# Performance work log

Hardware: AMD Instinct MI355X
Metric: run time of the kernel (lower is better)

## Reference

```python
import math
import jax, jax.numpy as jnp
import numpy as np

B, L, D, H = 4, 1024, 1024, 16
HD = D // H  # head_dim = 64


def rel_pos_embed(seq_len: int, dim: int, padding_idx: int = 0) -> jnp.ndarray:
    """RelativeSinusoidalPositionalEmbedding for seq_len > origin_shift case:
    table regenerated with num_embeddings = 2*seq_len, origin_shift = seq_len,
    positions = arange(-L, L) + L selects the full table. Returns [2L, dim]."""
    num = 2 * seq_len
    half = dim // 2
    scale = math.log(10000.0) / (half - 1)
    freq = np.exp(np.arange(half, dtype=np.float32) * -scale)
    pos = np.arange(-num // 2, num // 2, dtype=np.float32)
    emb = pos[:, None] * freq[None, :]                      # [2L, half]
    emb = np.concatenate([np.sin(emb), np.cos(emb)], axis=1).astype(np.float32)
    emb[padding_idx] = 0.0
    return jnp.asarray(emb)


def _shift(BD):
    """Transformer-XL shift: [b,n,L,2L] -> [b,n,L,L] aligning relative positions."""
    b, n, l, _ = BD.shape
    zero_pad = jnp.zeros((b, n, l, 1), BD.dtype)
    BD = jnp.concatenate([BD, zero_pad], axis=-1).reshape(b, n, -1, l)  # [b,n,2L+1,L]
    BD = BD[:, :, : 2 * l].reshape(b, n, l, -1)                          # [b,n,L,2L]
    return BD[..., l:]                                                    # [b,n,L,L]


def setup_inputs() -> dict:
    key = jax.random.key(0)
    k0, k1, k2, k3 = jax.random.split(key, 4)
    x = jax.random.normal(k0, (B, L, D), jnp.float32)
    Wqv = jax.random.normal(k1, (D, 2 * D), jnp.float32) * (1.0 / math.sqrt(D))
    r_r_bias = jax.random.normal(k2, (H, HD), jnp.float32) * 0.1
    r_w_bias = jax.random.normal(k3, (H, HD), jnp.float32) * 0.1
    mask = jnp.ones((B, L), jnp.int32)
    return {"x": x, "Wqv": Wqv, "r_r_bias": r_r_bias, "r_w_bias": r_w_bias, "mask": mask}


def reference(x, Wqv, r_r_bias, r_w_bias, mask):
    b, l, d = x.shape
    pos = rel_pos_embed(l, HD)                               # [2L, HD] (detached buffer)
    qv = x @ Wqv                                             # [b, L, 2D]
    q, v = jnp.split(qv, 2, axis=-1)
    q = q.reshape(b, l, H, HD).transpose(0, 2, 1, 3)         # [b, H, L, HD]
    v = v.reshape(b, l, H, HD).transpose(0, 2, 1, 3)
    k = x.reshape(b, l, H, HD).transpose(0, 2, 1, 3)         # k_as_x=True: k is x reshaped

    rw_head_q = q + r_r_bias[None, :, None, :]
    AC = jnp.einsum('bnqd,bnkd->bnqk', rw_head_q, k)         # [b,H,L,L]
    D_ = jnp.einsum('nd,ld->nl', r_w_bias, pos)[None, :, None, :]  # [1,H,1,2L]
    B_ = jnp.einsum('bnqd,ld->bnql', q, pos)                 # [b,H,L,2L]
    BD = _shift(B_ + D_)                                     # [b,H,L,L]

    attn = AC + BD
    attn = jnp.where(mask[:, None, None, :] == 0, -jnp.inf, attn)
    attn = jax.nn.softmax(attn, axis=-1)                     # dropout is identity (eval)
    out = jnp.einsum('bnqk,bnkd->bnqd', attn, v)
    return out.transpose(0, 2, 1, 3).reshape(b, l, d)
```

## Files before the change

### kernel.cpp

```cpp
#include <hip/hip_runtime.h>
#include <hip/hip_bf16.h>
#include <math.h>


typedef __attribute__((ext_vector_type(8))) short short8;
typedef __attribute__((ext_vector_type(4))) short short4v;
typedef __attribute__((ext_vector_type(4))) float f32x4;

#define MFMA16(a,b,c) __builtin_amdgcn_mfma_f32_16x16x32_bf16(a,b,c,0,0,0)

__device__ __forceinline__ short f2bf(float f) {
  union { float f; unsigned int u; } v; v.f = f;
  unsigned int u = v.u;
  u += 0x7FFFu + ((u >> 16) & 1u);
  return (short)(u >> 16);
}
__device__ __forceinline__ float bf2f(short h) {
  union { unsigned int u; float f; } v;
  v.u = ((unsigned int)(unsigned short)h) << 16;
  return v.f;
}
__device__ __forceinline__ void glds16(const short* g, short* l) {
  __builtin_amdgcn_global_load_lds(
      (const __attribute__((address_space(1))) void*)g,
      (__attribute__((address_space(3))) void*)l, 16, 0, 0);
}

__global__ __launch_bounds__(256) void k_trig(float* __restrict__ T) {
  int idx = blockIdx.x * 256 + threadIdx.x;
  int l = idx >> 6, c = idx & 63, cc = c & 31;
  float fr = (float)exp(-(double)cc * 0.2971077539347156);
  double ang = (double)l * (double)fr;
  T[idx] = (float)((c < 32) ? sin(ang) : cos(ang));
}

__global__ __launch_bounds__(256) void k_split_x(const float* __restrict__ x,
    short* __restrict__ xh, short* __restrict__ xl) {
  int i = blockIdx.x * 256 + threadIdx.x;
  f32x4 v = ((const f32x4*)x)[i];
  short4v h, l;
#pragma unroll
  for (int c = 0; c < 4; ++c) {
    short hb = f2bf(v[c]);
    h[c] = hb;
    l[c] = f2bf(v[c] - bf2f(hb));
  }
  ((short4v*)xh)[i] = h;
  ((short4v*)xl)[i] = l;
}

__global__ __launch_bounds__(256) void k_wt(const float* __restrict__ W,
    short* __restrict__ wth, short* __restrict__ wtl) {
  __shared__ __align__(16) float tile[64*65];
  int n0 = blockIdx.x * 64, k0 = blockIdx.y * 64;
  int tid = threadIdx.x;
#pragma unroll
  for (int i = 0; i < 16; ++i) {
    int e = tid + i*256, r = e >> 6, c = e & 63;
    tile[r*65 + c] = W[(k0 + r)*2048 + n0 + c];
  }
  __syncthreads();
#pragma unroll
  for (int i = 0; i < 16; ++i) {
    int e = tid + i*256, r = e >> 6, c = e & 63;
    float v = tile[c*65 + r];
    short hb = f2bf(v);
    wth[(n0 + r)*1024 + k0 + c] = hb;
    wtl[(n0 + r)*1024 + k0 + c] = f2bf(v - bf2f(hb));
  }
}

#define LDK 40
__global__ __launch_bounds__(256) void k_gemm(
    const short* __restrict__ xh, const short* __restrict__ xl,
    const short* __restrict__ wth, const short* __restrict__ wtl,
    float* __restrict__ qf, short* __restrict__ vbt) {
  __shared__ __align__(16) short Ah[128*LDK], Al[128*LDK], Bh[128*LDK], Bl[128*LDK];
  int tid = threadIdx.x;
  int m0 = blockIdx.x * 128, n0 = blockIdx.y * 128;
  int lane = tid & 63, w = tid >> 6;
  int wm = w >> 1, wn = w & 1;
  int g = lane >> 4, lr = lane & 15;
  f32x4 acc[4][4] = {};
  for (int kt = 0; kt < 32; ++kt) {
    int k0 = kt * 32;
#pragma unroll
    for (int i = 0; i < 2; ++i) {
      int L = tid + i*256;
      int r = L >> 2, c8 = (L & 3) * 8;
      *(short8*)&Ah[r*LDK + c8] = *(const short8*)&xh[(m0+r)*1024 + k0 + c8];
      *(short8*)&Al[r*LDK + c8] = *(const short8*)&xl[(m0+r)*1024 + k0 + c8];
      *(short8*)&Bh[r*LDK + c8] = *(const short8*)&wth[(n0+r)*1024 + k0 + c8];
      *(short8*)&Bl[r*LDK + c8] = *(const short8*)&wtl[(n0+r)*1024 + k0 + c8];
    }
    __syncthreads();
    short8 ah[4], al[4], bh[4], bl[4];
#pragma unroll
    for (int mf = 0; mf < 4; ++mf) {
      int row = wm*64 + mf*16 + lr;
      ah[mf] = *(short8*)&Ah[row*LDK + g*8];
      al[mf] = *(short8*)&Al[row*LDK + g*8];
    }
#pragma unroll
    for (int nf = 0; nf < 4; ++nf) {
      int row = wn*64 + nf*16 + lr;
      bh[nf] = *(short8*)&Bh[row*LDK + g*8];
      bl[nf] = *(short8*)&Bl[row*LDK + g*8];
    }
#pragma unroll
    for (int mf = 0; mf < 4; ++mf)
#pragma unroll
      for (int nf = 0; nf < 4; ++nf) {
        acc[mf][nf] = MFMA16(ah[mf], bh[nf], acc[mf][nf]);
        acc[mf][nf] = MFMA16(al[mf], bh[nf], acc[mf][nf]);
        acc[mf][nf] = MFMA16(ah[mf], bl[nf], acc[mf][nf]);
      }
    __syncthreads();
  }
#pragma unroll
  for (int mf = 0; mf < 4; ++mf)
#pragma unroll
    for (int nf = 0; nf < 4; ++nf) {
      int row0 = m0 + wm*64 + mf*16 + g*4;
      int col  = n0 + wn*64 + nf*16 + lr;
      if (col < 1024) {
#pragma unroll
        for (int ri = 0; ri < 4; ++ri)
          qf[(row0 + ri)*1024 + col] = acc[mf][nf][ri];
      } else {
        int c2 = col - 1024, h = c2 >> 6, d = c2 & 63;
        int b = row0 >> 10, l0 = row0 & 1023;
        short4v pk;
#pragma unroll
        for (int ri = 0; ri < 4; ++ri) pk[ri] = f2bf(acc[mf][nf][ri]);
        *(short4v*)&vbt[((b*16 + h)*64 + d)*1024 + l0] = pk;
      }
    }
}

__global__ __launch_bounds__(256) void k_qcat(const float* __restrict__ qf,
    const float* __restrict__ rrb, const float* __restrict__ rwb,
    const float* __restrict__ T, short* __restrict__ qch, short* __restrict__ qcl) {
  int row = blockIdx.x * 4 + (threadIdx.x >> 6);
  int lane = threadIdx.x & 63;
  int b = row >> 14, h = (row >> 10) & 15, l = row & 1023;
  float q  = qf[(b*1024 + l)*1024 + h*64 + lane];
  float qa = q + rrb[h*64 + lane];
  float qb = q + rwb[h*64 + lane];
  int c = lane & 31;
  float qs = __shfl(qb, c, 64);
  float qc = __shfl(qb, c + 32, 64);
  float ts = T[l*64 + c];
  float tc = T[l*64 + c + 32];
  float v2 = (lane < 32) ? (qs*tc + qc*ts) : (qc*tc - qs*ts);
  short ha = f2bf(qa), h2 = f2bf(v2);
  qch[row*128 + lane]      = ha;
  qcl[row*128 + lane]      = f2bf(qa - bf2f(ha));
  qch[row*128 + 64 + lane] = h2;
  qcl[row*128 + 64 + lane] = f2bf(v2 - bf2f(h2));
}

__global__ __launch_bounds__(256) void k_kcat(const float* __restrict__ x,
    const float* __restrict__ T, short* __restrict__ kch, short* __restrict__ kcl) {
  int row = blockIdx.x * 4 + (threadIdx.x >> 6);
  int lane = threadIdx.x & 63;
  int b = row >> 14, h = (row >> 10) & 15, k = row & 1023;
  float xv = x[(b*1024 + k)*1024 + h*64 + lane];
  float tv = T[k*64 + lane];
  short hx = f2bf(xv), ht = f2bf(tv);
  int sw = k & 7;
  int c0 = lane, c1 = 64 + lane;
  int p0 = ((((c0 >> 3) ^ sw) << 3) | (c0 & 7));
  int p1 = ((((c1 >> 3) ^ sw) << 3) | (c1 & 7));
  kch[row*128 + p0] = hx;
  kcl[row*128 + p0] = f2bf(xv - bf2f(hx));
  kch[row*128 + p1] = ht;
  kcl[row*128 + p1] = f2bf(tv - bf2f(ht));
}

#define NKT 32
#define PLDW 40
__global__ __launch_bounds__(512, 4) void k_attn(
    const short* __restrict__ qch, const short* __restrict__ qcl,
    const short* __restrict__ kch, const short* __restrict__ kcl,
    const short* __restrict__ vbt, float* __restrict__ out) {
  __shared__ __align__(16) short Kh[2][32*128], Kl[2][32*128], Pl[8][16*PLDW];
  int tid = threadIdx.x, lane = tid & 63, w = tid >> 6;
  int g = lane >> 4, lr = lane & 15;
  int id = blockIdx.x;
  int s = id >> 3, xcd = id & 7;
  int bh = xcd*8 + (s & 7), qt = s >> 3;
  int q0 = qt * 128;
  short8 qh[4], ql[4];
  int qrow = bh*1024 + q0 + w*16 + lr;
#pragma unroll
  for (int kc = 0; kc < 4; ++kc) {
    qh[kc] = *(const short8*)&qch[qrow*128 + kc*32 + g*8];
    ql[kc] = *(const short8*)&qcl[qrow*128 + kc*32 + g*8];
  }
  f32x4 o[4] = {};
  float m_run[4], l_run[4];
#pragma unroll
  for (int r = 0; r < 4; ++r) { m_run[r] = -1e30f; l_run[r] = 0.f; }
  short* Pw = &Pl[w][0];
  glds16(&kch[(bh*1024)*128 + tid*8], &Kh[0][tid*8]);
  glds16(&kcl[(bh*1024)*128 + tid*8], &Kl[0][tid*8]);
  __syncthreads();
  for (int kt = 0; kt < NKT; ++kt) {
    int cur = kt & 1;
    short8 vb[4];
#pragma unroll
    for (int df = 0; df < 4; ++df)
      vb[df] = *(const short8*)&vbt[(bh*64 + df*16 + lr)*1024 + kt*32 + g*8];
    if (kt + 1 < NKT) {
      int off = (bh*1024 + (kt+1)*32)*128;
      glds16(&kch[off + tid*8], &Kh[cur^1][tid*8]);
      glds16(&kcl[off + tid*8], &Kl[cur^1][tid*8]);
    }
    f32x4 sacc[2] = {};
#pragma unroll
    for (int kc = 0; kc < 4; ++kc)
#pragma unroll
      for (int nf = 0; nf < 2; ++nf) {
        int boff = (nf*16 + lr)*256 + ((((kc<<2) + g) ^ (lr & 7)) << 4);
        short8 kbh = *(short8*)((char*)&Kh[cur][0] + boff);
        short8 kbl = *(short8*)((char*)&Kl[cur][0] + boff);
        sacc[nf] = MFMA16(qh[kc], kbh, sacc[nf]);
        sacc[nf] = MFMA16(ql[kc], kbh, sacc[nf]);
        sacc[nf] = MFMA16(qh[kc], kbl, sacc[nf]);
      }
    float mt[4];
#pragma unroll
    for (int r = 0; r < 4; ++r) mt[r] = fmaxf(sacc[0][r], sacc[1][r]);
#pragma unroll
    for (int off = 1; off < 16; off <<= 1)
#pragma unroll
      for (int r = 0; r < 4; ++r)
        mt[r] = fmaxf(mt[r], __shfl_xor(mt[r], off, 64));
    float sc[4], rs[4];
#pragma unroll
    for (int r = 0; r < 4; ++r) {
      float mn = fmaxf(m_run[r], mt[r]);
      sc[r] = __expf(m_run[r] - mn);
      m_run[r] = mn;
      rs[r] = 0.f;
    }
#pragma unroll
    for (int nf = 0; nf < 2; ++nf)
#pragma unroll
      for (int r = 0; r < 4; ++r) {
        float p = __expf(sacc[nf][r] - m_run[r]);
        rs[r] += p;
        Pw[(g*4 + r)*PLDW + nf*16 + lr] = f2bf(p);
      }
#pragma unroll
    for (int off = 1; off < 16; off <<= 1)
#pragma unroll
      for (int r = 0; r < 4; ++r)
        rs[r] += __shfl_xor(rs[r], off, 64);
#pragma unroll
    for (int r = 0; r < 4; ++r) l_run[r] = l_run[r]*sc[r] + rs[r];
#pragma unroll
    for (int df = 0; df < 4; ++df)
#pragma unroll
      for (int r = 0; r < 4; ++r)
        o[df][r] *= sc[r];
    short8 pa = *(short8*)&Pw[lr*PLDW + g*8];
#pragma unroll
    for (int df = 0; df < 4; ++df)
      o[df] = MFMA16(pa, vb[df], o[df]);
    __syncthreads();
  }
  int b = bh >> 4, h = bh & 15;
#pragma unroll
  for (int df = 0; df < 4; ++df)
#pragma unroll
    for (int r = 0; r < 4; ++r) {
      int qa = q0 + w*16 + g*4 + r;
      out[(b*1024 + qa)*1024 + h*64 + df*16 + lr] = o[df][r] / l_run[r];
    }
}

extern "C" void kernel_launch(void* const* d_in, const int* in_sizes, int n_in,
                              void* d_out, int out_size, void* d_ws, size_t ws_size,
                              hipStream_t stream) {
  const float* x   = (const float*)d_in[0];
  const float* Wqv = (const float*)d_in[1];
  const float* rrb = (const float*)d_in[2];
  const float* rwb = (const float*)d_in[3];
  float* out = (float*)d_out;
  char* ws = (char*)d_ws;
  const size_t MB = 1u << 20;
  float* T   = (float*)(ws);
  short* vbt = (short*)(ws + 1*MB);
  short* qch = (short*)(ws + 9*MB);
  short* qcl = (short*)(ws + 25*MB);
  short* kch = (short*)(ws + 41*MB);
  short* kcl = (short*)(ws + 57*MB);
  short* xh  = (short*)(ws + 41*MB);
  short* xl  = (short*)(ws + 49*MB);
  short* wth = (short*)(ws + 57*MB);
  short* wtl = (short*)(ws + 61*MB);
  float* qf  = (float*)d_out;

  hipLaunchKernelGGL(k_trig,   dim3(256),      dim3(256), 0, stream, T);
  hipLaunchKernelGGL(k_split_x,dim3(4096),     dim3(256), 0, stream, x, xh, xl);
  hipLaunchKernelGGL(k_wt,     dim3(32, 16),   dim3(256), 0, stream, Wqv, wth, wtl);
  hipLaunchKernelGGL(k_gemm,   dim3(32, 16),   dim3(256), 0, stream, xh, xl, wth, wtl, qf, vbt);
  hipLaunchKernelGGL(k_qcat,   dim3(16384),    dim3(256), 0, stream, qf, rrb, rwb, T, qch, qcl);
  hipLaunchKernelGGL(k_kcat,   dim3(16384),    dim3(256), 0, stream, x, T, kch, kcl);
  hipLaunchKernelGGL(k_attn,   dim3(512),      dim3(512), 0, stream, qch, qcl, kch, kcl, vbt, out);
}
```

Before: 283.4 us.

## Double query rows per wave in attention, lazy rescale, MFMA rowsum, direct LDS loads

The attention kernel now runs 4 waves per block, and each wave handles two 16-row query tiles, so every K fragment read from LDS feeds twice as many MFMAs. Online-softmax rescaling is skipped unless the running max grows by more than a threshold. Row sums are accumulated through an extra MFMA against a ones vector instead of shuffle reductions. The GEMM uses global_load_lds for staging with an unpadded LDS layout, and both kernels raise wave priority around MFMA blocks. The risks are higher register pressure, possible LDS bank conflicts in the unpadded GEMM tiles, and a larger range for the bf16 probabilities.

```diff
diff --git a/kernel.cpp b/kernel.cpp
--- a/kernel.cpp
+++ b/kernel.cpp
@@ -70,12 +70,11 @@
   }
 }
 
-#define LDK 40
 __global__ __launch_bounds__(256) void k_gemm(
     const short* __restrict__ xh, const short* __restrict__ xl,
     const short* __restrict__ wth, const short* __restrict__ wtl,
     float* __restrict__ qf, short* __restrict__ vbt) {
-  __shared__ __align__(16) short Ah[128*LDK], Al[128*LDK], Bh[128*LDK], Bl[128*LDK];
+  __shared__ __align__(16) short Ah[128*32], Al[128*32], Bh[128*32], Bl[128*32];
   int tid = threadIdx.x;
   int m0 = blockIdx.x * 128, n0 = blockIdx.y * 128;
   int lane = tid & 63, w = tid >> 6;
@@ -85,28 +84,29 @@
   for (int kt = 0; kt < 32; ++kt) {
     int k0 = kt * 32;
 #pragma unroll
-    for (int i = 0; i < 2; ++i) {
-      int L = tid + i*256;
-      int r = L >> 2, c8 = (L & 3) * 8;
-      *(short8*)&Ah[r*LDK + c8] = *(const short8*)&xh[(m0+r)*1024 + k0 + c8];
-      *(short8*)&Al[r*LDK + c8] = *(const short8*)&xl[(m0+r)*1024 + k0 + c8];
-      *(short8*)&Bh[r*LDK + c8] = *(const short8*)&wth[(n0+r)*1024 + k0 + c8];
-      *(short8*)&Bl[r*LDK + c8] = *(const short8*)&wtl[(n0+r)*1024 + k0 + c8];
+    for (int p = 0; p < 2; ++p) {
+      int e = p*256 + tid;
+      int r = e >> 2, c8 = (e & 3) * 8, e8 = e * 8;
+      glds16(&xh [(m0+r)*1024 + k0 + c8], &Ah[e8]);
+      glds16(&xl [(m0+r)*1024 + k0 + c8], &Al[e8]);
+      glds16(&wth[(n0+r)*1024 + k0 + c8], &Bh[e8]);
+      glds16(&wtl[(n0+r)*1024 + k0 + c8], &Bl[e8]);
     }
     __syncthreads();
     short8 ah[4], al[4], bh[4], bl[4];
 #pragma unroll
     for (int mf = 0; mf < 4; ++mf) {
       int row = wm*64 + mf*16 + lr;
-      ah[mf] = *(short8*)&Ah[row*LDK + g*8];
-      al[mf] = *(short8*)&Al[row*LDK + g*8];
+      ah[mf] = *(short8*)&Ah[row*32 + g*8];
+      al[mf] = *(short8*)&Al[row*32 + g*8];
     }
 #pragma unroll
     for (int nf = 0; nf < 4; ++nf) {
       int row = wn*64 + nf*16 + lr;
-      bh[nf] = *(short8*)&Bh[row*LDK + g*8];
-      bl[nf] = *(short8*)&Bl[row*LDK + g*8];
-    }
+      bh[nf] = *(short8*)&Bh[row*32 + g*8];
+      bl[nf] = *(short8*)&Bl[row*32 + g*8];
+    }
+    __builtin_amdgcn_s_setprio(1);
 #pragma unroll
     for (int mf = 0; mf < 4; ++mf)
 #pragma unroll
@@ -115,6 +115,7 @@
         acc[mf][nf] = MFMA16(al[mf], bh[nf], acc[mf][nf]);
         acc[mf][nf] = MFMA16(ah[mf], bl[nf], acc[mf][nf]);
       }
+    __builtin_amdgcn_s_setprio(0);
     __syncthreads();
   }
 #pragma unroll
@@ -180,31 +181,43 @@
 
 #define NKT 32
 #define PLDW 40
-__global__ __launch_bounds__(512, 4) void k_attn(
+__global__ __launch_bounds__(256, 2) void k_attn(
     const short* __restrict__ qch, const short* __restrict__ qcl,
     const short* __restrict__ kch, const short* __restrict__ kcl,
     const short* __restrict__ vbt, float* __restrict__ out) {
-  __shared__ __align__(16) short Kh[2][32*128], Kl[2][32*128], Pl[8][16*PLDW];
+  __shared__ __align__(16) short Kh[2][32*128], Kl[2][32*128];
+  __shared__ __align__(16) short Pl[4][2][16*PLDW];
   int tid = threadIdx.x, lane = tid & 63, w = tid >> 6;
   int g = lane >> 4, lr = lane & 15;
   int id = blockIdx.x;
   int s = id >> 3, xcd = id & 7;
   int bh = xcd*8 + (s & 7), qt = s >> 3;
   int q0 = qt * 128;
-  short8 qh[4], ql[4];
-  int qrow = bh*1024 + q0 + w*16 + lr;
-#pragma unroll
-  for (int kc = 0; kc < 4; ++kc) {
-    qh[kc] = *(const short8*)&qch[qrow*128 + kc*32 + g*8];
-    ql[kc] = *(const short8*)&qcl[qrow*128 + kc*32 + g*8];
-  }
-  f32x4 o[4] = {};
-  float m_run[4], l_run[4];
-#pragma unroll
-  for (int r = 0; r < 4; ++r) { m_run[r] = -1e30f; l_run[r] = 0.f; }
-  short* Pw = &Pl[w][0];
-  glds16(&kch[(bh*1024)*128 + tid*8], &Kh[0][tid*8]);
-  glds16(&kcl[(bh*1024)*128 + tid*8], &Kl[0][tid*8]);
+  short8 qh[2][4], ql[2][4];
+#pragma unroll
+  for (int m = 0; m < 2; ++m) {
+    int qrow = bh*1024 + q0 + w*32 + m*16 + lr;
+#pragma unroll
+    for (int kc = 0; kc < 4; ++kc) {
+      qh[m][kc] = *(const short8*)&qch[qrow*128 + kc*32 + g*8];
+      ql[m][kc] = *(const short8*)&qcl[qrow*128 + kc*32 + g*8];
+    }
+  }
+  f32x4 o[2][5] = {};
+  float m_run[2][4];
+#pragma unroll
+  for (int m = 0; m < 2; ++m)
+#pragma unroll
+    for (int r = 0; r < 4; ++r) m_run[m][r] = -1e30f;
+  short8 onesv;
+#pragma unroll
+  for (int i = 0; i < 8; ++i) onesv[i] = (short)0x3F80;
+#pragma unroll
+  for (int p = 0; p < 2; ++p) {
+    int e8 = (p*256 + tid) * 8;
+    glds16(&kch[(bh*1024)*128 + e8], &Kh[0][e8]);
+    glds16(&kcl[(bh*1024)*128 + e8], &Kl[0][e8]);
+  }
   __syncthreads();
   for (int kt = 0; kt < NKT; ++kt) {
     int cur = kt & 1;
@@ -214,10 +227,15 @@
       vb[df] = *(const short8*)&vbt[(bh*64 + df*16 + lr)*1024 + kt*32 + g*8];
     if (kt + 1 < NKT) {
       int off = (bh*1024 + (kt+1)*32)*128;
-      glds16(&kch[off + tid*8], &Kh[cur^1][tid*8]);
-      glds16(&kcl[off + tid*8], &Kl[cur^1][tid*8]);
-    }
-    f32x4 sacc[2] = {};
+#pragma unroll
+      for (int p = 0; p < 2; ++p) {
+        int e8 = (p*256 + tid) * 8;
+        glds16(&kch[off + e8], &Kh[cur^1][e8]);
+        glds16(&kcl[off + e8], &Kl[cur^1][e8]);
+      }
+    }
+    f32x4 sacc[2][2] = {};
+    __builtin_amdgcn_s_setprio(1);
 #pragma unroll
     for (int kc = 0; kc < 4; ++kc)
 #pragma unroll
@@ -225,60 +243,76 @@
         int boff = (nf*16 + lr)*256 + ((((kc<<2) + g) ^ (lr & 7)) << 4);
         short8 kbh = *(short8*)((char*)&Kh[cur][0] + boff);
         short8 kbl = *(short8*)((char*)&Kl[cur][0] + boff);
-        sacc[nf] = MFMA16(qh[kc], kbh, sacc[nf]);
-        sacc[nf] = MFMA16(ql[kc], kbh, sacc[nf]);
-        sacc[nf] = MFMA16(qh[kc], kbl, sacc[nf]);
-      }
-    float mt[4];
-#pragma unroll
-    for (int r = 0; r < 4; ++r) mt[r] = fmaxf(sacc[0][r], sacc[1][r]);
+#pragma unroll
+        for (int m = 0; m < 2; ++m) {
+          sacc[m][nf] = MFMA16(qh[m][kc], kbh, sacc[m][nf]);
+          sacc[m][nf] = MFMA16(ql[m][kc], kbh, sacc[m][nf]);
+          sacc[m][nf] = MFMA16(qh[m][kc], kbl, sacc[m][nf]);
+        }
+      }
+    __builtin_amdgcn_s_setprio(0);
+    float mt[2][4];
+#pragma unroll
+    for (int m = 0; m < 2; ++m)
+#pragma unroll
+      for (int r = 0; r < 4; ++r)
+        mt[m][r] = fmaxf(sacc[m][0][r], sacc[m][1][r]);
 #pragma unroll
     for (int off = 1; off < 16; off <<= 1)
 #pragma unroll
+      for (int m = 0; m < 2; ++m)
+#pragma unroll
+        for (int r = 0; r < 4; ++r)
+          mt[m][r] = fmaxf(mt[m][r], __shfl_xor(mt[m][r], off, 64));
+    float dmax = mt[0][0] - m_run[0][0];
+#pragma unroll
+    for (int m = 0; m < 2; ++m)
+#pragma unroll
       for (int r = 0; r < 4; ++r)
-        mt[r] = fmaxf(mt[r], __shfl_xor(mt[r], off, 64));
-    float sc[4], rs[4];
-#pragma unroll
-    for (int r = 0; r < 4; ++r) {
-      float mn = fmaxf(m_run[r], mt[r]);
-      sc[r] = __expf(m_run[r] - mn);
-      m_run[r] = mn;
-      rs[r] = 0.f;
-    }
-#pragma unroll
-    for (int nf = 0; nf < 2; ++nf)
+        dmax = fmaxf(dmax, mt[m][r] - m_run[m][r]);
+    if (!__all(dmax <= 8.0f)) {
+#pragma unroll
+      for (int m = 0; m < 2; ++m)
+#pragma unroll
+        for (int r = 0; r < 4; ++r) {
+          float mn = fmaxf(m_run[m][r], mt[m][r]);
+          float sc = __expf(m_run[m][r] - mn);
+          m_run[m][r] = mn;
+#pragma unroll
+          for (int df = 0; df < 5; ++df) o[m][df][r] *= sc;
+        }
+    }
+#pragma unroll
+    for (int m = 0; m < 2; ++m)
+#pragma unroll
+      for (int nf = 0; nf < 2; ++nf)
+#pragma unroll
+        for (int r = 0; r < 4; ++r) {
+          float p = __expf(sacc[m][nf][r] - m_run[m][r]);
+          Pl[w][m][(g*4 + r)*PLDW + nf*16 + lr] = f2bf(p);
+        }
+    __builtin_amdgcn_s_setprio(1);
+#pragma unroll
+    for (int m = 0; m < 2; ++m) {
+      short8 pa = *(short8*)&Pl[w][m][lr*PLDW + g*8];
+#pragma unroll
+      for (int df = 0; df < 4; ++df)
+        o[m][df] = MFMA16(pa, vb[df], o[m][df]);
+      o[m][4] = MFMA16(pa, onesv, o[m][4]);
+    }
+    __builtin_amdgcn_s_setprio(0);
+    __syncthreads();
+  }
+  int b = bh >> 4, h = bh & 15;
+#pragma unroll
+  for (int m = 0; m < 2; ++m)
+#pragma unroll
+    for (int df = 0; df < 4; ++df)
 #pragma unroll
       for (int r = 0; r < 4; ++r) {
-        float p = __expf(sacc[nf][r] - m_run[r]);
-        rs[r] += p;
-        Pw[(g*4 + r)*PLDW + nf*16 + lr] = f2bf(p);
-      }
-#pragma unroll
-    for (int off = 1; off < 16; off <<= 1)
-#pragma unroll
-      for (int r = 0; r < 4; ++r)
-        rs[r] += __shfl_xor(rs[r], off, 64);
-#pragma unroll
-    for (int r = 0; r < 4; ++r) l_run[r] = l_run[r]*sc[r] + rs[r];
-#pragma unroll
-    for (int df = 0; df < 4; ++df)
-#pragma unroll
-      for (int r = 0; r < 4; ++r)
-        o[df][r] *= sc[r];
-    short8 pa = *(short8*)&Pw[lr*PLDW + g*8];
-#pragma unroll
-    for (int df = 0; df < 4; ++df)
-      o[df] = MFMA16(pa, vb[df], o[df]);
-    __syncthreads();
-  }
-  int b = bh >> 4, h = bh & 15;
-#pragma unroll
-  for (int df = 0; df < 4; ++df)
-#pragma unroll
-    for (int r = 0; r < 4; ++r) {
-      int qa = q0 + w*16 + g*4 + r;
-      out[(b*1024 + qa)*1024 + h*64 + df*16 + lr] = o[df][r] / l_run[r];
-    }
+        int qa = q0 + w*32 + m*16 + g*4 + r;
+        out[(b*1024 + qa)*1024 + h*64 + df*16 + lr] = o[m][df][r] / o[m][4][r];
+      }
 }
 
 extern "C" void kernel_launch(void* const* d_in, const int* in_sizes, int n_in,
@@ -309,5 +343,5 @@
   hipLaunchKernelGGL(k_gemm,   dim3(32, 16),   dim3(256), 0, stream, xh, xl, wth, wtl, qf, vbt);
   hipLaunchKernelGGL(k_qcat,   dim3(16384),    dim3(256), 0, stream, qf, rrb, rwb, T, qch, qcl);
   hipLaunchKernelGGL(k_kcat,   dim3(16384),    dim3(256), 0, stream, x, T, kch, kcl);
-  hipLaunchKernelGGL(k_attn,   dim3(512),      dim3(512), 0, stream, qch, qcl, kch, kcl, vbt, out);
-}
+  hipLaunchKernelGGL(k_attn,   dim3(512),      dim3(256), 0, stream, qch, qcl, kch, kcl, vbt, out);
+}
```

Result: faster. 249.2 us (-12.1%).
